# Performance work log

Hardware: AMD Instinct MI355X
Metric: run time of the kernel (lower is better)

## Reference

```python
import jax, jax.numpy as jnp
import numpy as np

N_GENES = 15135
N_CMT = 1000
HID = 64


def _gcn_norm(edge_index, n):
    # add self-loops, compute symmetric normalization deg^-1/2 * deg^-1/2
    loop = jnp.arange(n, dtype=edge_index.dtype)
    src = jnp.concatenate([edge_index[0], loop])
    dst = jnp.concatenate([edge_index[1], loop])
    deg = jax.ops.segment_sum(jnp.ones_like(src, dtype=jnp.float32), dst, num_segments=n)
    dinv = jnp.where(deg > 0, 1.0 / jnp.sqrt(deg), 0.0)
    return src, dst, dinv[src] * dinv[dst]


def _gcn_conv(x, W, b, src, dst, norm, n):
    h = x @ W                                  # [bs, N, H]
    m = h[:, src, :] * norm[None, :, None]     # gather messages [bs, E, H]
    out = jnp.zeros_like(h).at[:, dst, :].add(m)
    return out + b


def setup_inputs():
    key = jax.random.key(0)
    ks = jax.random.split(key, 16)
    bs, nf, hfc, ncls, E, P = 8, 64, 128, 2, 242160, 120000
    s = 0.05
    return {
        "x": jax.random.normal(ks[0], (bs, N_GENES, nf), jnp.float32),
        "batch": jnp.zeros((bs,), jnp.int32),
        "edge_index": jax.random.randint(ks[1], (2, E), 0, N_GENES),
        "path_row": jax.random.randint(ks[2], (P,), 0, N_GENES),
        "path_col": jax.random.randint(ks[3], (P,), 0, N_CMT),
        "W1": jax.random.normal(ks[4], (nf, HID), jnp.float32) * s,
        "b1": jnp.zeros((HID,), jnp.float32),
        "W2": jax.random.normal(ks[5], (HID, HID), jnp.float32) * s,
        "b2": jnp.zeros((HID,), jnp.float32),
        "W3": jax.random.normal(ks[6], (HID, HID), jnp.float32) * s,
        "b3": jnp.zeros((HID,), jnp.float32),
        "fcW": jax.random.normal(ks[7], (3 * HID, 1), jnp.float32) * s,
        "fcb": jnp.zeros((1,), jnp.float32),
        "l1W": jax.random.normal(ks[8], (N_CMT, hfc), jnp.float32) * s,
        "l1b": jnp.zeros((hfc,), jnp.float32),
        "l2W": jax.random.normal(ks[9], (hfc, ncls), jnp.float32) * s,
        "l2b": jnp.zeros((ncls,), jnp.float32),
    }


def reference(x, batch, edge_index, path_row, path_col,
              W1, b1, W2, b2, W3, b3, fcW, fcb, l1W, l1b, l2W, l2b):
    bs, n = x.shape[0], x.shape[1]
    src, dst, norm = _gcn_norm(edge_index, n)

    x1 = jax.nn.relu(_gcn_conv(x, W1, b1, src, dst, norm, n))
    x2 = jax.nn.relu(_gcn_conv(x1, W2, b2, src, dst, norm, n))
    x3 = jax.nn.relu(_gcn_conv(x2, W3, b3, src, dst, norm, n))
    # mode='cat': torch.stack(xs, -1).view(bs, N, -1) -> layout [..., h*L + l]
    xc = jnp.stack([x1, x2, x3], axis=-1).reshape(bs, n, HID * 3)

    # pathway pooling: scatter_mean(x[row], col) over node axis
    xt = jnp.transpose(xc, (1, 0, 2))            # [N, bs, F]
    g = xt[path_row]                             # [P, bs, F]
    sums = jax.ops.segment_sum(g, path_col, num_segments=N_CMT)
    cnt = jax.ops.segment_sum(jnp.ones_like(path_col, dtype=xc.dtype), path_col, num_segments=N_CMT)
    pooled = sums / jnp.maximum(cnt, 1.0)[:, None, None]   # [n_cmt, bs, F]
    pooled = jnp.transpose(pooled, (1, 0, 2)).reshape(-1, HID * 3)  # [bs*n_cmt, F]

    h = (pooled @ fcW + fcb).reshape(bs, N_CMT)   # fc -> view(-1, n_cmt)
    h = jax.nn.relu(h @ l1W + l1b)                # (dropout is identity in eval)
    h = h @ l2W + l2b
    return jax.nn.log_softmax(h, axis=-1)
```

## Files before the change

kernel.cpp:

```cpp
#include <hip/hip_runtime.h>
#include <hip/hip_bf16.h>
#include <hip/hip_fp16.h>
#include <math.h>

#define HID 64

#if defined(__has_builtin)
#if __has_builtin(__builtin_amdgcn_cvt_pk_f32_fp8) && __has_builtin(__builtin_amdgcn_cvt_pk_fp8_f32)
#define HWFP8 1
#endif
#endif

typedef float vfloat2 __attribute__((ext_vector_type(2)));
typedef __attribute__((ext_vector_type(8))) short short8_t;
typedef __attribute__((ext_vector_type(4))) float f32x4;

union ABFrag { short8_t s; unsigned short u[8]; };


__device__ __forceinline__ unsigned short f2bf(float x) {
    unsigned int u = __float_as_uint(x);
    unsigned int r = u + 0x7fffu + ((u >> 16) & 1u);
    return (unsigned short)(r >> 16);
}

#ifndef HWFP8
__device__ __forceinline__ unsigned int enc8_sw(float a) {
    unsigned short hb = __half_as_ushort(__float2half(a));
    unsigned int r = (unsigned int)hb + 0x7fu + ((hb >> 8) & 1u);
    return (r >> 8) & 0xffu;
}
__device__ __forceinline__ float dec8_sw(unsigned int b) {
    return __half2float(__ushort_as_half((unsigned short)(b << 8)));
}
#endif

__device__ __forceinline__ unsigned int enc4(float a, float b, float c, float d) {
#ifdef HWFP8
    int r = __builtin_amdgcn_cvt_pk_fp8_f32(a, b, 0, false);
    r = __builtin_amdgcn_cvt_pk_fp8_f32(c, d, r, true);
    return (unsigned int)r;
#else
    return enc8_sw(a) | (enc8_sw(b) << 8) | (enc8_sw(c) << 16) | (enc8_sw(d) << 24);
#endif
}

__device__ __forceinline__ void dec4(unsigned int w, float* f) {
#ifdef HWFP8
    vfloat2 a = __builtin_amdgcn_cvt_pk_f32_fp8((int)w, false);
    vfloat2 b = __builtin_amdgcn_cvt_pk_f32_fp8((int)w, true);
    f[0] = a.x; f[1] = a.y; f[2] = b.x; f[3] = b.y;
#else
    f[0] = dec8_sw(w & 0xffu); f[1] = dec8_sw((w >> 8) & 0xffu);
    f[2] = dec8_sw((w >> 16) & 0xffu); f[3] = dec8_sw(w >> 24);
#endif
}

__device__ __forceinline__ void dec8(uint2 g, float* f) {
    dec4(g.x, f);
    dec4(g.y, f + 4);
}

__device__ __forceinline__ void gemm_epilogue(float* so, const f32x4* acc,
                                              unsigned int* Yq, float S,
                                              int r0w, int rowsTot, int lane) {
    int cc = lane & 15;
    int cr = (lane >> 4) * 4;
#pragma unroll
    for (int c = 0; c < 4; ++c) {
        so[(cr + 0) * 68 + c * 16 + cc] = acc[c][0];
        so[(cr + 1) * 68 + c * 16 + cc] = acc[c][1];
        so[(cr + 2) * 68 + c * 16 + cc] = acc[c][2];
        so[(cr + 3) * 68 + c * 16 + cc] = acc[c][3];
    }
    __syncthreads();
#pragma unroll
    for (int i = 0; i < 4; ++i) {
        int idx = lane + i * 64;
        int row = idx >> 4, ci = idx & 15;
        int grow = r0w + row;
        if (grow < rowsTot) {
            float4 v = *(const float4*)&so[row * 68 + ci * 4];
            Yq[(size_t)grow * 16 + ci] = enc4(v.x * S, v.y * S, v.z * S, v.w * S);
        }
    }
}

__global__ __launch_bounds__(256) void k_fused1(const float* __restrict__ x,
                                                const float* __restrict__ W1,
                                                unsigned int* __restrict__ Yq,
                                                float S, int N, int rowsTot, int gGf,
                                                const int* __restrict__ edst, int* __restrict__ deg, int E,
                                                const int* __restrict__ pcol, int* __restrict__ ccnt, int P,
                                                const float* __restrict__ W2, const float* __restrict__ W3,
                                                unsigned short* __restrict__ Wt) {
    __shared__ float sOut[4][16 * 68];
    __shared__ unsigned short sW[4096];
    int tid = threadIdx.x;
    if ((int)blockIdx.x < gGf) {
        int w = tid >> 6, lane = tid & 63;
        int cc = lane & 15, kg = (lane >> 4) * 8;
        float* so = &sOut[w][0];
#pragma unroll
        for (int i = 0; i < 16; ++i) {
            int idx = i * 256 + tid;
            int k = idx >> 6, c = idx & 63;
            sW[c * 64 + k] = f2bf(W1[idx]);
        }
        __syncthreads();
        ABFrag bf[2][4];
#pragma unroll
        for (int h = 0; h < 2; ++h)
#pragma unroll
            for (int c = 0; c < 4; ++c)
                bf[h][c].s = *(const short8_t*)&sW[(c * 16 + cc) * 64 + h * 32 + kg];

        int base = blockIdx.x * 128;
        ABFrag a[2];
        auto loadA = [&](int rA, ABFrag* dst) {
#pragma unroll
            for (int h = 0; h < 2; ++h) {
                if (rA < rowsTot) {
                    int n = rA >> 3, b = rA & 7;
                    const float* p = &x[((size_t)b * N + n) * 64 + h * 32 + kg];
                    float4 v0 = *(const float4*)p;
                    float4 v1 = *(const float4*)(p + 4);
                    dst[h].u[0] = f2bf(v0.x); dst[h].u[1] = f2bf(v0.y);
                    dst[h].u[2] = f2bf(v0.z); dst[h].u[3] = f2bf(v0.w);
                    dst[h].u[4] = f2bf(v1.x); dst[h].u[5] = f2bf(v1.y);
                    dst[h].u[6] = f2bf(v1.z); dst[h].u[7] = f2bf(v1.w);
                } else {
#pragma unroll
                    for (int j = 0; j < 8; ++j) dst[h].u[j] = 0;
                }
            }
        };
        loadA(base + w * 16 + (lane & 15), a);
#pragma unroll
        for (int t = 0; t < 2; ++t) {
            ABFrag an[2];
            if (t < 1) loadA(base + 64 + w * 16 + (lane & 15), an);
            f32x4 acc[4] = {f32x4{}, f32x4{}, f32x4{}, f32x4{}};
#pragma unroll
            for (int h = 0; h < 2; ++h)
#pragma unroll
                for (int c = 0; c < 4; ++c)
                    acc[c] = __builtin_amdgcn_mfma_f32_16x16x32_bf16(a[h].s, bf[h][c].s, acc[c], 0, 0, 0);
            gemm_epilogue(so, acc, Yq, S, base + t * 64 + w * 16, rowsTot, lane);
            if (t < 1) { a[0] = an[0]; a[1] = an[1]; __syncthreads(); }
        }
    } else {
        int cb = blockIdx.x - gGf;
        int nCB = gridDim.x - gGf;
        int gth = cb * 256 + tid;
        int GT = nCB * 256;
        for (int e = gth; e < E; e += GT) atomicAdd(&deg[edst[e]], 1);
        for (int p = gth; p < P; p += GT) atomicAdd(&ccnt[pcol[p]], 1);
        for (int i = gth; i < 2 * 4096; i += GT) {
            int l = i >> 12, r = i & 4095;
            int k = r >> 6, c = r & 63;
            const float* W = (l == 0) ? W2 : W3;
            Wt[(l << 12) + c * 64 + k] = f2bf(W[r]);
        }
    }
}


__global__ __launch_bounds__(256) void k_pre_scan(const int* __restrict__ deg, int* __restrict__ rowoff, int N,
                                                  const int* __restrict__ ccnt, int* __restrict__ coff, int NC,
                                                  float* __restrict__ dinv) {
    __shared__ int part[256];
    int t = threadIdx.x;
    int gth = blockIdx.x * blockDim.x + t;
    int GT = gridDim.x * blockDim.x;
    for (int i = gth; i < N; i += GT) dinv[i] = rsqrtf((float)(deg[i] + 1));

    const int* cnt = nullptr; int* off = nullptr; int n = 0;
    if (blockIdx.x == 0)      { cnt = deg;  off = rowoff; n = N; }
    else if (blockIdx.x == 1) { cnt = ccnt; off = coff;   n = NC; }
    else return;

    int CH = (n + 255) >> 8;
    int lo = min(t * CH, n), hi = min(lo + CH, n);
    int sum = 0;
    for (int i = lo; i < hi; ++i) sum += cnt[i];
    part[t] = sum;
    __syncthreads();
    for (int o = 1; o < 256; o <<= 1) {
        int v = (t >= o) ? part[t - o] : 0;
        __syncthreads();
        part[t] += v;
        __syncthreads();
    }
    int run = (t == 0) ? 0 : part[t - 1];
    for (int i = lo; i < hi; ++i) { off[i] = run; run += cnt[i]; }
    if (t == 255) off[n] = run;
}

__global__ __launch_bounds__(256) void k_pre_scatter(const int* __restrict__ esrc, const int* __restrict__ edst,
                                                     const float* __restrict__ dinv, const int* __restrict__ rowoff,
                                                     int* __restrict__ fill, int* __restrict__ ssrc,
                                                     float* __restrict__ snorm, int E,
                                                     const int* __restrict__ prow, const int* __restrict__ pcol,
                                                     const int* __restrict__ coff, int* __restrict__ cfill,
                                                     int* __restrict__ crow, int P) {
    int gth = blockIdx.x * blockDim.x + threadIdx.x;
    int GT = gridDim.x * blockDim.x;
    for (int e = gth; e < E; e += GT) {
        int s = esrc[e], d = edst[e];
        int pos = rowoff[d] + atomicAdd(&fill[d], 1);
        ssrc[pos]  = s;
        snorm[pos] = dinv[s] * dinv[d];
    }
    for (int p = gth; p < P; p += GT) {
        int c = pcol[p];
        int pos = coff[c] + atomicAdd(&cfill[c], 1);
        crow[pos] = prow[p];
    }
}

template<int LAYER>
__device__ __forceinline__ void agg_node(const uint2* __restrict__ Y,
                                         const int* __restrict__ rowoff,
                                         const int* __restrict__ ssrc,
                                         const float* __restrict__ snorm,
                                         const float* __restrict__ dinv,
                                         const float* bv, const float* wv,
                                         float* __restrict__ sArr,
                                         float invS, int n, int lane,
                                         float* accOut) {
    float dn = dinv[n];
    float w0 = dn * dn;
    int beg = rowoff[n], end = rowoff[n + 1];

    uint2 gs = Y[(size_t)n * 64 + lane];
    float acc[8] = {0.f, 0.f, 0.f, 0.f, 0.f, 0.f, 0.f, 0.f};
    float f[8];
    bool haveSelf = false;

    for (int i = beg; i < end; i += 8) {
        int   sI[8];
        float wI[8];
        uint2 g[8];
#pragma unroll
        for (int u = 0; u < 8; ++u) {
            int valid = (i + u < end);
            int idx = valid ? (i + u) : i;
            sI[u] = ssrc[idx];
            wI[u] = valid ? snorm[idx] : 0.f;
        }
#pragma unroll
        for (int u = 0; u < 8; ++u) g[u] = Y[(size_t)sI[u] * 64 + lane];
        if (!haveSelf) {
            dec8(gs, f);
#pragma unroll
            for (int k = 0; k < 8; ++k) acc[k] = w0 * f[k];
            haveSelf = true;
        }
#pragma unroll
        for (int u = 0; u < 8; ++u) {
            dec8(g[u], f);
#pragma unroll
            for (int k = 0; k < 8; ++k) acc[k] = fmaf(wI[u], f[k], acc[k]);
        }
    }
    if (!haveSelf) {
        dec8(gs, f);
#pragma unroll
        for (int k = 0; k < 8; ++k) acc[k] = w0 * f[k];
    }

    float sv = 0.f;
#pragma unroll
    for (int k = 0; k < 8; ++k) {
        float o = fmaxf(fmaf(acc[k], invS, bv[k]), 0.f);
        accOut[k] = o;
        sv = fmaf(o, wv[k], sv);
    }
    sv += __shfl_down(sv, 4, 64);
    sv += __shfl_down(sv, 2, 64);
    sv += __shfl_down(sv, 1, 64);
    if ((lane & 7) == 0) {
        int b = lane >> 3;
        float* sp = sArr + (size_t)n * 8 + b;
        if (LAYER == 0) *sp = sv;
        else            *sp += sv;
    }
}

template<int LAYER>
__global__ __launch_bounds__(256) void k_aggemm(const uint2* __restrict__ Yin,
                                                const int* __restrict__ rowoff,
                                                const int* __restrict__ ssrc,
                                                const float* __restrict__ snorm,
                                                const float* __restrict__ dinv,
                                                const float* __restrict__ bias,
                                                const float* __restrict__ fcW,
                                                float* __restrict__ sArr, float invS,
                                                const unsigned short* __restrict__ Wt,
                                                unsigned int* __restrict__ Yout, float Sout,
                                                int N, int rowsTot) {
    struct ShU { union { unsigned short sX[64 * 64]; float sOut[4][16 * 68]; }; };
    __shared__ ShU sh;
    int tid = threadIdx.x;
    int w = tid >> 6, lane = tid & 63;
    int b = lane >> 3, hb = (lane & 7) * 8;

    float bv[8], wv[8];
#pragma unroll
    for (int k = 0; k < 8; ++k) { bv[k] = bias[hb + k]; wv[k] = fcW[3 * (hb + k) + LAYER]; }

    int n0 = blockIdx.x * 8;
#pragma unroll
    for (int j = 0; j < 2; ++j) {
        int ln = w * 2 + j;
        int n = n0 + ln;
        int r = ln * 8 + b;
        unsigned int byte = (unsigned int)(r * 128 + hb * 2) ^ ((unsigned int)(r & 7) << 4);
        short8_t* dst = (short8_t*)((char*)sh.sX + byte);
        if (n < N) {
            float acc[8];
            agg_node<LAYER>(Yin, rowoff, ssrc, snorm, dinv, bv, wv, sArr, invS, n, lane, acc);
            ABFrag xr;
#pragma unroll
            for (int k = 0; k < 8; ++k) xr.u[k] = f2bf(acc[k]);
            *dst = xr.s;
        } else {
            ABFrag xr;
#pragma unroll
            for (int k = 0; k < 8; ++k) xr.u[k] = 0;
            *dst = xr.s;
        }
    }
    __syncthreads();

    int cc = lane & 15, kg = (lane >> 4) * 8;
    ABFrag bf[2][4];
#pragma unroll
    for (int h = 0; h < 2; ++h)
#pragma unroll
        for (int c = 0; c < 4; ++c)
            bf[h][c].s = *(const short8_t*)&Wt[(size_t)(c * 16 + cc) * 64 + h * 32 + kg];

    int rA = w * 16 + (lane & 15);
    ABFrag a[2];
#pragma unroll
    for (int h = 0; h < 2; ++h) {
        unsigned int byte = (unsigned int)(rA * 128 + (h * 32 + kg) * 2) ^ ((unsigned int)(rA & 7) << 4);
        a[h].s = *(const short8_t*)((const char*)sh.sX + byte);
    }
    f32x4 acc4[4] = {f32x4{}, f32x4{}, f32x4{}, f32x4{}};
#pragma unroll
    for (int h = 0; h < 2; ++h)
#pragma unroll
        for (int c = 0; c < 4; ++c)
            acc4[c] = __builtin_amdgcn_mfma_f32_16x16x32_bf16(a[h].s, bf[h][c].s, acc4[c], 0, 0, 0);
    __syncthreads();
    gemm_epilogue(&sh.sOut[w][0], acc4, Yout, Sout, blockIdx.x * 64 + w * 16, rowsTot, lane);
}


template<int LAYER>
__global__ __launch_bounds__(256) void k_agg(const uint2* __restrict__ Y,
                                             const int* __restrict__ rowoff,
                                             const int* __restrict__ ssrc,
                                             const float* __restrict__ snorm,
                                             const float* __restrict__ dinv,
                                             const float* __restrict__ bias,
                                             const float* __restrict__ fcW,
                                             float* __restrict__ sArr,
                                             float invS, int N) {
    int n = blockIdx.x * 4 + (threadIdx.x >> 6);
    if (n >= N) return;
    int lane = threadIdx.x & 63;
    int hb = (lane & 7) * 8;
    float bv[8], wv[8];
#pragma unroll
    for (int k = 0; k < 8; ++k) { bv[k] = bias[hb + k]; wv[k] = fcW[3 * (hb + k) + LAYER]; }
    float acc[8];
    agg_node<LAYER>(Y, rowoff, ssrc, snorm, dinv, bv, wv, sArr, invS, n, lane, acc);
}


__global__ __launch_bounds__(128) void k_l1pool(const float* __restrict__ sArr,
                                                const int* __restrict__ coff,
                                                const int* __restrict__ crow,
                                                const float* __restrict__ fcb,
                                                const float* __restrict__ l1W,
                                                float* __restrict__ hpre,
                                                int* __restrict__ done,
                                                const float* __restrict__ l1b,
                                                const float* __restrict__ l2W,
                                                const float* __restrict__ l2b,
                                                float* __restrict__ out,
                                                int NC, int HFC, int bs, int NCLS,
                                                int CHUNK, int nBlocks) {
    __shared__ float hl[64];
    int b = blockIdx.y;
    int c0 = blockIdx.x * CHUNK;
    int j = threadIdx.x;
    int cend = min(c0 + CHUNK, NC);
    {
        int w = j >> 6, lane = j & 63, q = lane >> 4, s = lane & 15;
        float fcb0 = fcb[0];
        for (int c = c0 + w * 4 + q; c < cend; c += 8) {
            int beg = coff[c], end = coff[c + 1];
            float acc = 0.f;
            for (int i = beg + s; i < end; i += 16)
                acc += sArr[(size_t)crow[i] * 8 + b];
            acc += __shfl_down(acc, 8, 16);
            acc += __shfl_down(acc, 4, 16);
            acc += __shfl_down(acc, 2, 16);
            acc += __shfl_down(acc, 1, 16);
            if (s == 0)
                hl[c - c0] = acc / fmaxf((float)(end - beg), 1.f) + fcb0;
        }
    }
    __syncthreads();
    float acc = 0.f;
    for (int c = c0; c < cend; ++c) acc = fmaf(hl[c - c0], l1W[(size_t)c * HFC + j], acc);
    atomicAdd(&hpre[(size_t)b * HFC + j], acc);

    __threadfence();
    __syncthreads();
    __shared__ int amLast;
    if (j == 0) amLast = (atomicAdd(done, 1) == nBlocks - 1);
    __syncthreads();
    if (!amLast) return;
    __threadfence();

    __shared__ float sZ[64];
    int g = j >> 3, l8 = j & 7;
    int nout = bs * NCLS;
    float v = 0.f;
    int b2 = g / NCLS, k2 = g - b2 * NCLS;
    if (g < nout) {
        for (int jj = l8; jj < HFC; jj += 8) {
            float h = fmaxf(hpre[(size_t)b2 * HFC + jj] + l1b[jj], 0.f);
            v = fmaf(h, l2W[(size_t)jj * NCLS + k2], v);
        }
    }
    v += __shfl_down(v, 4, 8);
    v += __shfl_down(v, 2, 8);
    v += __shfl_down(v, 1, 8);
    if (l8 == 0 && g < nout) sZ[g] = v + l2b[k2];
    __syncthreads();
    if (j < bs) {
        float m = -1e30f;
        for (int c = 0; c < NCLS; ++c) m = fmaxf(m, sZ[j * NCLS + c]);
        float s = 0.f;
        for (int c = 0; c < NCLS; ++c) s += expf(sZ[j * NCLS + c] - m);
        float lse = m + logf(s);
        for (int c = 0; c < NCLS; ++c) out[j * NCLS + c] = sZ[j * NCLS + c] - lse;
    }
}


extern "C" void kernel_launch(void* const* d_in, const int* in_sizes, int n_in,
                              void* d_out, int out_size, void* d_ws, size_t ws_size,
                              hipStream_t stream) {
    const float* x   = (const float*)d_in[0];
    const int* eidx  = (const int*)d_in[2];
    const int* prow  = (const int*)d_in[3];
    const int* pcol  = (const int*)d_in[4];
    const float* W1  = (const float*)d_in[5];
    const float* b1  = (const float*)d_in[6];
    const float* W2  = (const float*)d_in[7];
    const float* b2  = (const float*)d_in[8];
    const float* W3  = (const float*)d_in[9];
    const float* b3  = (const float*)d_in[10];
    const float* fcW = (const float*)d_in[11];
    const float* fcb = (const float*)d_in[12];
    const float* l1W = (const float*)d_in[13];
    const float* l1b = (const float*)d_in[14];
    const float* l2W = (const float*)d_in[15];
    const float* l2b = (const float*)d_in[16];
    float* out = (float*)d_out;

    const int bs   = in_sizes[1];
    const int E    = in_sizes[2] / 2;
    const int P    = in_sizes[3];
    const int N    = in_sizes[0] / (bs * HID);
    const int HFC  = in_sizes[14];
    const int NC   = in_sizes[13] / HFC;
    const int NCLS = in_sizes[15] / HFC;
    const int rows = N * bs;

    const int* esrc = eidx;
    const int* edst = eidx + E;

    size_t off = 0;
    auto alloc = [&](size_t bytes) -> void* {
        void* r = (char*)d_ws + off;
        off += (bytes + 255) & ~(size_t)255;
        return r;
    };
    char* zbase   = (char*)d_ws;
    int*   deg    = (int*)  alloc((size_t)N * 4);
    int*   fill   = (int*)  alloc((size_t)N * 4);
    int*   ccnt   = (int*)  alloc((size_t)NC * 4);
    int*   cfill  = (int*)  alloc((size_t)NC * 4);
    float* hpre   = (float*)alloc((size_t)bs * HFC * 4);
    int*   done   = (int*)  alloc(4);
    size_t zspan  = off;
    float* dinv   = (float*)alloc((size_t)N * 4);
    int*   rowoff = (int*)  alloc(((size_t)N + 1) * 4);
    int*   coff   = (int*)  alloc(((size_t)NC + 1) * 4);
    int*   crow   = (int*)  alloc((size_t)P * 4);
    int*   ssrc   = (int*)  alloc((size_t)E * 4);
    float* snorm  = (float*)alloc((size_t)E * 4);
    unsigned int* Yqa  = (unsigned int*)alloc((size_t)rows * HID);
    unsigned int* Yqb  = (unsigned int*)alloc((size_t)rows * HID);
    float* sArr   = (float*)alloc((size_t)rows * 4);
    unsigned short* Wt = (unsigned short*)alloc((size_t)2 * 64 * 64 * 2);

    hipMemsetAsync(zbase, 0, zspan, stream);

    const float S1 = 1.f,  iS1 = 1.f;
    const float S2 = 16.f, iS2 = 1.f / 16.f;
    const float S3 = 128.f, iS3 = 1.f / 128.f;

    int gG2 = (rows + 127) / 128;
    int gF  = (N + 7) / 8;
    int gA  = (N + 3) / 4;
    int gPre = 512;

    k_fused1<<<gG2 + gPre, 256, 0, stream>>>(x, W1, Yqa, S1, N, rows, gG2,
                                             edst, deg, E, pcol, ccnt, P, W2, W3, Wt);
    k_pre_scan<<<64, 256, 0, stream>>>(deg, rowoff, N, ccnt, coff, NC, dinv);
    k_pre_scatter<<<gPre, 256, 0, stream>>>(esrc, edst, dinv, rowoff, fill, ssrc, snorm, E,
                                            prow, pcol, coff, cfill, crow, P);

    k_aggemm<0><<<gF, 256, 0, stream>>>((const uint2*)Yqa, rowoff, ssrc, snorm, dinv, b1, fcW,
                                        sArr, iS1, Wt, Yqb, S2, N, rows);
    k_aggemm<1><<<gF, 256, 0, stream>>>((const uint2*)Yqb, rowoff, ssrc, snorm, dinv, b2, fcW,
                                        sArr, iS2, Wt + 4096, Yqa, S3, N, rows);
    k_agg<2><<<gA, 256, 0, stream>>>((const uint2*)Yqa, rowoff, ssrc, snorm, dinv, b3, fcW,
                                     sArr, iS3, N);

    const int CHUNK = 40;
    dim3 gL1((NC + CHUNK - 1) / CHUNK, bs);
    int nBlocks = gL1.x * gL1.y;
    k_l1pool<<<gL1, 128, 0, stream>>>(sArr, coff, crow, fcb, l1W, hpre, done,
                                      l1b, l2W, l2b, out, NC, HFC, bs, NCLS, CHUNK, nBlocks);
}
```

Baseline: 341.9 us.

## Split pathway pooling into its own kernel computing all batches per pathway

Pathway mean pooling moves out of the fused L1 kernel into a new kernel with one wavefront per pathway, where the 8 lanes in each group cover the 8 batch entries of the same sArr row. Each crow index therefore feeds a contiguous 32-byte read instead of being re-gathered once per batch block, and the loop is unrolled by four to keep more loads in flight. The L1 kernel then reads pooled values from a small intermediate buffer. This adds one kernel launch and a round trip through global memory for the intermediate.

```diff
diff --git a/kernel.cpp b/kernel.cpp
--- a/kernel.cpp
+++ b/kernel.cpp
@@ -218,6 +218,7 @@
         crow[pos] = prow[p];
     }
 }
+
 
 template<int LAYER>
 __device__ __forceinline__ void agg_node(const uint2* __restrict__ Y,
@@ -382,40 +383,53 @@
 }
 
 
-__global__ __launch_bounds__(128) void k_l1pool(const float* __restrict__ sArr,
-                                                const int* __restrict__ coff,
-                                                const int* __restrict__ crow,
-                                                const float* __restrict__ fcb,
-                                                const float* __restrict__ l1W,
-                                                float* __restrict__ hpre,
-                                                int* __restrict__ done,
-                                                const float* __restrict__ l1b,
-                                                const float* __restrict__ l2W,
-                                                const float* __restrict__ l2b,
-                                                float* __restrict__ out,
-                                                int NC, int HFC, int bs, int NCLS,
-                                                int CHUNK, int nBlocks) {
+__global__ __launch_bounds__(64) void k_poolg(const float* __restrict__ sArr,
+                                              const int* __restrict__ coff,
+                                              const int* __restrict__ crow,
+                                              float* __restrict__ hpoolT) {
+    int c = blockIdx.x;
+    int lane = threadIdx.x;
+    int beg = coff[c], end = coff[c + 1];
+    int b = lane & 7;
+    float acc = 0.f;
+    int i = beg + (lane >> 3);
+    for (; i + 24 < end; i += 32) {
+        int r0 = crow[i], r1 = crow[i + 8], r2 = crow[i + 16], r3 = crow[i + 24];
+        float a0 = sArr[(size_t)r0 * 8 + b];
+        float a1 = sArr[(size_t)r1 * 8 + b];
+        float a2 = sArr[(size_t)r2 * 8 + b];
+        float a3 = sArr[(size_t)r3 * 8 + b];
+        acc += (a0 + a1) + (a2 + a3);
+    }
+    for (; i < end; i += 8) acc += sArr[(size_t)crow[i] * 8 + b];
+    acc += __shfl_down(acc, 32, 64);
+    acc += __shfl_down(acc, 16, 64);
+    acc += __shfl_down(acc, 8, 64);
+    if (lane < 8) {
+        float inv = 1.f / fmaxf((float)(end - beg), 1.f);
+        hpoolT[(size_t)c * 8 + b] = acc * inv;
+    }
+}
+
+
+__global__ __launch_bounds__(128) void k_l1f(const float* __restrict__ hpoolT,
+                                             const float* __restrict__ fcb,
+                                             const float* __restrict__ l1W,
+                                             float* __restrict__ hpre,
+                                             int* __restrict__ done,
+                                             const float* __restrict__ l1b,
+                                             const float* __restrict__ l2W,
+                                             const float* __restrict__ l2b,
+                                             float* __restrict__ out,
+                                             int NC, int HFC, int bs, int NCLS,
+                                             int CHUNK, int nBlocks) {
     __shared__ float hl[64];
     int b = blockIdx.y;
     int c0 = blockIdx.x * CHUNK;
     int j = threadIdx.x;
     int cend = min(c0 + CHUNK, NC);
-    {
-        int w = j >> 6, lane = j & 63, q = lane >> 4, s = lane & 15;
-        float fcb0 = fcb[0];
-        for (int c = c0 + w * 4 + q; c < cend; c += 8) {
-            int beg = coff[c], end = coff[c + 1];
-            float acc = 0.f;
-            for (int i = beg + s; i < end; i += 16)
-                acc += sArr[(size_t)crow[i] * 8 + b];
-            acc += __shfl_down(acc, 8, 16);
-            acc += __shfl_down(acc, 4, 16);
-            acc += __shfl_down(acc, 2, 16);
-            acc += __shfl_down(acc, 1, 16);
-            if (s == 0)
-                hl[c - c0] = acc / fmaxf((float)(end - beg), 1.f) + fcb0;
-        }
-    }
+    for (int c = c0 + j; c < cend; c += blockDim.x)
+        hl[c - c0] = hpoolT[(size_t)c * 8 + b] + fcb[0];
     __syncthreads();
     float acc = 0.f;
     for (int c = c0; c < cend; ++c) acc = fmaf(hl[c - c0], l1W[(size_t)c * HFC + j], acc);
@@ -507,6 +521,7 @@
     int*   rowoff = (int*)  alloc(((size_t)N + 1) * 4);
     int*   coff   = (int*)  alloc(((size_t)NC + 1) * 4);
     int*   crow   = (int*)  alloc((size_t)P * 4);
+    float* hpoolT = (float*)alloc((size_t)NC * bs * 4);
     int*   ssrc   = (int*)  alloc((size_t)E * 4);
     float* snorm  = (float*)alloc((size_t)E * 4);
     unsigned int* Yqa  = (unsigned int*)alloc((size_t)rows * HID);
@@ -538,9 +553,11 @@
     k_agg<2><<<gA, 256, 0, stream>>>((const uint2*)Yqa, rowoff, ssrc, snorm, dinv, b3, fcW,
                                      sArr, iS3, N);
 
+    k_poolg<<<NC, 64, 0, stream>>>(sArr, coff, crow, hpoolT);
+
     const int CHUNK = 40;
     dim3 gL1((NC + CHUNK - 1) / CHUNK, bs);
     int nBlocks = gL1.x * gL1.y;
-    k_l1pool<<<gL1, 128, 0, stream>>>(sArr, coff, crow, fcb, l1W, hpre, done,
-                                      l1b, l2W, l2b, out, NC, HFC, bs, NCLS, CHUNK, nBlocks);
-}
+    k_l1f<<<gL1, 128, 0, stream>>>(hpoolT, fcb, l1W, hpre, done, l1b, l2W, l2b, out,
+                                   NC, HFC, bs, NCLS, CHUNK, nBlocks);
+}
```

New measurement: 327.1 us. 4.3% less time.
